# Performance work log

Hardware: AMD Instinct MI355X
Metric: run time of the kernel (lower is better)

Reference implementation:

```python
import jax, jax.numpy as jnp
import numpy as np

EMBED_DIM = 1024
B, T = 4, 2048

def setup_inputs() -> dict:
    key = jax.random.key(0)
    ks = jax.random.split(key, 7)
    s = 1.0 / np.sqrt(EMBED_DIM)
    return {
        "x": jax.random.normal(ks[0], (B, T, EMBED_DIM), dtype=jnp.float32),
        "Wq": jax.random.uniform(ks[1], (EMBED_DIM, EMBED_DIM), jnp.float32, -s, s),
        "bq": jax.random.uniform(ks[2], (EMBED_DIM,), jnp.float32, -s, s),
        "Wk": jax.random.uniform(ks[3], (EMBED_DIM, EMBED_DIM), jnp.float32, -s, s),
        "bk": jax.random.uniform(ks[4], (EMBED_DIM,), jnp.float32, -s, s),
        "Wv": jax.random.uniform(ks[5], (EMBED_DIM, EMBED_DIM), jnp.float32, -s, s),
        "bv": jax.random.uniform(ks[6], (EMBED_DIM,), jnp.float32, -s, s),
    }

def reference(x, Wq, bq, Wk, bk, Wv, bv):
    Bsz, Tlen, C = x.shape
    # torch Linear: y = x @ W.T + b
    Q = jnp.einsum('btc,dc->btd', x, Wq) + bq
    K = jnp.einsum('btc,dc->btd', x, Wk) + bk
    V = jnp.einsum('btc,dc->btd', x, Wv) + bv
    score = jnp.einsum('bqd,bkd->bqk', Q, K) / jnp.sqrt(jnp.float32(C))
    causal = jnp.tril(jnp.ones((Tlen, Tlen), dtype=bool))  # [T,T]
    score = jnp.where(causal, score, -jnp.inf)
    att = jax.nn.softmax(score, axis=-1)
    return jnp.einsum('bqk,bkd->bqd', att, V)
```

## Files before the change

### kernel.cpp

```cpp
#include <hip/hip_runtime.h>


using u16 = unsigned short;
typedef __attribute__((ext_vector_type(8))) short short8;
typedef __attribute__((ext_vector_type(4))) float f32x4;

__device__ __forceinline__ u16 f2b(float f) {
  unsigned u = __builtin_bit_cast(unsigned, f);
  u += 0x7fffu + ((u >> 16) & 1u);
  return (u16)(u >> 16);
}

__device__ __forceinline__ float b2f(u16 h) {
  return __builtin_bit_cast(float, (unsigned)h << 16);
}

__device__ __forceinline__ void async16(void* lds, const void* g) {
  __builtin_amdgcn_global_load_lds(
      (const __attribute__((address_space(1))) unsigned int*)g,
      (__attribute__((address_space(3))) unsigned int*)lds, 16, 0, 0);
}

__global__ __launch_bounds__(256) void cvt_all_kernel(
    const float* __restrict__ x, const float* __restrict__ Wq,
    const float* __restrict__ Wk, const float* __restrict__ Wv,
    u16* __restrict__ xb, u16* __restrict__ Wcat) {
  const int i = blockIdx.x * 256 + threadIdx.x;
  const float* src;
  u16* dst;
  int c;
  if (i < 2097152) {
    src = x; dst = xb; c = i;
  } else {
    const int r = i - 2097152;
    const int seg = r >> 18;
    src = seg == 0 ? Wq : (seg == 1 ? Wk : Wv);
    dst = Wcat + (size_t)seg * 1048576;
    c = r & 262143;
  }
  const float4 v = reinterpret_cast<const float4*>(src)[c];
  ushort4 o;
  o.x = f2b(v.x); o.y = f2b(v.y); o.z = f2b(v.z); o.w = f2b(v.w);
  reinterpret_cast<ushort4*>(dst)[c] = o;
}

template <typename Epi>
__device__ __forceinline__ void gemm_bt_tile(const u16* __restrict__ A, int lda,
                                             const u16* __restrict__ B, int ldb,
                                             int nt, Epi&& epi) {
  __shared__ __align__(16) u16 As[128 * 64];
  __shared__ __align__(16) u16 Bs[128 * 64];
  const int tid = threadIdx.x;
  const int lane = tid & 63;
  const int w = tid >> 6;
  const int wr = (w >> 1) << 6;
  const int wc = (w & 1) << 6;

  f32x4 acc[4][4];
#pragma unroll
  for (int i = 0; i < 4; ++i)
#pragma unroll
    for (int j = 0; j < 4; ++j) acc[i][j] = f32x4{0.f, 0.f, 0.f, 0.f};

  const int sr = tid >> 3;
  const int ce = ((tid & 7) ^ (sr & 7)) << 3;
  const u16* gA = A + (size_t)sr * lda + ce;
  const u16* gB = B + (size_t)sr * ldb + ce;
  u16* const dA = As + tid * 8;
  u16* const dB = Bs + tid * 8;

  const int hi = lane >> 4;
  const int lo7 = lane & 7;
  const int ra = (wr + (lane & 15)) << 6;
  const int rb = (wc + (lane & 15)) << 6;
  const int sk0 = (hi ^ lo7) << 3;
  const int sk1 = ((4 + hi) ^ lo7) << 3;

  for (int t = 0; t < nt; ++t) {
    __syncthreads();
#pragma unroll
    for (int s = 0; s < 4; ++s) {
      async16(dA + s * 2048, gA + (size_t)(s * 32) * lda);
      async16(dB + s * 2048, gB + (size_t)(s * 32) * ldb);
    }
    gA += 64;
    gB += 64;
    __syncthreads();
#pragma unroll
    for (int kk = 0; kk < 2; ++kk) {
      const int sk = kk ? sk1 : sk0;
      short8 af[4], bf[4];
#pragma unroll
      for (int i = 0; i < 4; ++i)
        af[i] = *(const short8*)(As + ra + i * 1024 + sk);
#pragma unroll
      for (int j = 0; j < 4; ++j)
        bf[j] = *(const short8*)(Bs + rb + j * 1024 + sk);
#pragma unroll
      for (int i = 0; i < 4; ++i)
#pragma unroll
        for (int j = 0; j < 4; ++j)
          acc[i][j] = __builtin_amdgcn_mfma_f32_16x16x32_bf16(af[i], bf[j],
                                                              acc[i][j], 0, 0, 0);
    }
  }
  epi(acc, wr, wc, lane);
}

__global__ __launch_bounds__(256) void qkv_kernel(
    const u16* __restrict__ xb, const u16* __restrict__ Wcat,
    const float* __restrict__ bq, const float* __restrict__ bk,
    const float* __restrict__ bv, u16* __restrict__ Qb, u16* __restrict__ Kb,
    u16* __restrict__ Vtb) {
  const int bid = blockIdx.x;
  const int z = bid >> 9;
  const int r = bid & 511;
  if (z < 2) {
    const int mt = r >> 3, nt = r & 7;
    const u16* W = Wcat + (size_t)z * 1048576;
    const float* bias = z ? bk : bq;
    u16* out = z ? Kb : Qb;
    const float scale = z ? 1.0f : 0.03125f;
    gemm_bt_tile(
        xb + (size_t)mt * 128 * 1024, 1024, W + (size_t)nt * 128 * 1024, 1024, 16,
        [&](f32x4(&acc)[4][4], int wr, int wc, int lane) {
          const int r0 = mt * 128 + wr + ((lane >> 4) << 2);
          const int c0 = nt * 128 + wc + (lane & 15);
#pragma unroll
          for (int i = 0; i < 4; ++i)
#pragma unroll
            for (int j = 0; j < 4; ++j) {
              const int col = c0 + j * 16;
              const float bb = bias[col];
#pragma unroll
              for (int rr = 0; rr < 4; ++rr)
                out[(size_t)(r0 + i * 16 + rr) * 1024 + col] =
                    f2b((acc[i][j][rr] + bb) * scale);
            }
        });
  } else {
    const int mt = r >> 6, nt = r & 63;
    const u16* Wvb = Wcat + (size_t)2 * 1048576;
    gemm_bt_tile(
        Wvb + (size_t)mt * 128 * 1024, 1024, xb + (size_t)nt * 128 * 1024, 1024, 16,
        [&](f32x4(&acc)[4][4], int wr, int wc, int lane) {
          const int r0 = mt * 128 + wr + ((lane >> 4) << 2);
          const int c0 = nt * 128 + wc + (lane & 15);
#pragma unroll
          for (int i = 0; i < 4; ++i)
#pragma unroll
            for (int rr = 0; rr < 4; ++rr) {
              const int row = r0 + i * 16 + rr;
              const float bb = bv[row];
#pragma unroll
              for (int j = 0; j < 4; ++j)
                Vtb[(size_t)row * 8192 + c0 + j * 16] = f2b(acc[i][j][rr] + bb);
            }
        });
  }
}

__global__ __launch_bounds__(256) void score_kernel(const u16* __restrict__ Qb,
                                                    const u16* __restrict__ Kb,
                                                    u16* __restrict__ S) {
  const int b = blockIdx.y;
  const int t = blockIdx.x;
  int qt = 0;
  while ((qt + 1) * (qt + 2) / 2 <= t) ++qt;
  const int kt = t - (qt * (qt + 1)) / 2;
  const u16* A = Qb + ((size_t)b * 2048 + qt * 128) * 1024;
  const u16* Bp = Kb + ((size_t)b * 2048 + kt * 128) * 1024;
  u16* Sb = S + (size_t)b * 2048 * 2048;
  gemm_bt_tile(A, 1024, Bp, 1024, 16,
               [&](f32x4(&acc)[4][4], int wr, int wc, int lane) {
                 const int r0 = qt * 128 + wr + ((lane >> 4) << 2);
                 const int c0 = kt * 128 + wc + (lane & 15);
#pragma unroll
                 for (int i = 0; i < 4; ++i)
#pragma unroll
                   for (int j = 0; j < 4; ++j)
#pragma unroll
                     for (int rr = 0; rr < 4; ++rr)
                       Sb[(size_t)(r0 + i * 16 + rr) * 2048 + c0 + j * 16] =
                           f2b(acc[i][j][rr]);
               });
}

__global__ __launch_bounds__(256) void softmax_kernel(const u16* __restrict__ S,
                                                      u16* __restrict__ P) {
  __shared__ float redm[4], reds[4];
  const int rowid = blockIdx.x;
  const int b = rowid >> 11;
  const int q = rowid & 2047;
  const u16* Srow = S + ((size_t)b * 2048 + q) * 2048;
  u16* Prow = P + ((size_t)b * 2048 + q) * 2048;
  const int L = q + 1;
  const int Lpad = ((q >> 7) + 1) << 7;
  const int tid = threadIdx.x;
  const int k0 = tid << 3;
  const bool active = k0 < Lpad;
  float v[8];
  float m = -1e30f;
  if (active) {
    const short8 s8 = *(const short8*)(Srow + k0);
#pragma unroll
    for (int j = 0; j < 8; ++j) {
      v[j] = (k0 + j < L) ? b2f((u16)s8[j]) : -1e30f;
      m = fmaxf(m, v[j]);
    }
  }
#pragma unroll
  for (int o = 32; o > 0; o >>= 1) m = fmaxf(m, __shfl_xor(m, o));
  if ((tid & 63) == 0) redm[tid >> 6] = m;
  __syncthreads();
  m = fmaxf(fmaxf(redm[0], redm[1]), fmaxf(redm[2], redm[3]));
  float s = 0.f;
  if (active) {
#pragma unroll
    for (int j = 0; j < 8; ++j) {
      const float e = (k0 + j < L) ? __expf(v[j] - m) : 0.f;
      v[j] = e;
      s += e;
    }
  }
#pragma unroll
  for (int o = 32; o > 0; o >>= 1) s += __shfl_xor(s, o);
  if ((tid & 63) == 0) reds[tid >> 6] = s;
  __syncthreads();
  s = reds[0] + reds[1] + reds[2] + reds[3];
  const float inv = 1.0f / s;
  if (active) {
    short8 o8;
#pragma unroll
    for (int j = 0; j < 8; ++j)
      o8[j] = (short)((k0 + j < L) ? f2b(v[j] * inv) : (u16)0);
    *(short8*)(Prow + k0) = o8;
  }
}

__global__ __launch_bounds__(256) void pv_kernel(const u16* __restrict__ P,
                                                 const u16* __restrict__ Vtb,
                                                 float* __restrict__ O) {
  const int bid = blockIdx.x;
  const int pair = bid >> 8;
  const int idx = bid & 255;
  const int hb = idx >> 7;
  const int qt_raw = (idx >> 3) & 15;
  const int dt = idx & 7;
  const int qt = pair ? (15 - qt_raw) : qt_raw;
  const int b = pair * 2 + hb;
  const u16* A = P + (size_t)b * 2048 * 2048 + (size_t)qt * 128 * 2048;
  const u16* Bp = Vtb + (size_t)dt * 128 * 8192 + b * 2048;
  float* Ob = O + (size_t)b * 2048 * 1024;
  gemm_bt_tile(A, 2048, Bp, 8192, (qt + 1) * 2,
               [&](f32x4(&acc)[4][4], int wr, int wc, int lane) {
                 const int r0 = qt * 128 + wr + ((lane >> 4) << 2);
                 const int c0 = dt * 128 + wc + (lane & 15);
#pragma unroll
                 for (int i = 0; i < 4; ++i)
#pragma unroll
                   for (int j = 0; j < 4; ++j)
#pragma unroll
                     for (int rr = 0; rr < 4; ++rr)
                       Ob[(size_t)(r0 + i * 16 + rr) * 1024 + c0 + j * 16] =
                           acc[i][j][rr];
               });
}

extern "C" void kernel_launch(void* const* d_in, const int* in_sizes, int n_in,
                              void* d_out, int out_size, void* d_ws, size_t ws_size,
                              hipStream_t stream) {
  const float* x = (const float*)d_in[0];
  const float* Wq = (const float*)d_in[1];
  const float* bq = (const float*)d_in[2];
  const float* Wk = (const float*)d_in[3];
  const float* bk = (const float*)d_in[4];
  const float* Wv = (const float*)d_in[5];
  const float* bv = (const float*)d_in[6];
  float* out = (float*)d_out;
  char* ws = (char*)d_ws;
  u16* Qb = (u16*)(ws);
  u16* Kb = (u16*)(ws + (16u << 20));
  u16* Vtb = (u16*)(ws + (32u << 20));
  u16* xb = (u16*)(ws + (48u << 20));
  u16* Wcat = (u16*)(ws + (64u << 20));
  u16* S = (u16*)(ws + (70u << 20));
  u16* P = (u16*)(ws + (134u << 20));

  cvt_all_kernel<<<11264, 256, 0, stream>>>(x, Wq, Wk, Wv, xb, Wcat);
  qkv_kernel<<<1536, 256, 0, stream>>>(xb, Wcat, bq, bk, bv, Qb, Kb, Vtb);
  score_kernel<<<dim3(136, 4), 256, 0, stream>>>(Qb, Kb, S);
  softmax_kernel<<<8192, 256, 0, stream>>>(S, P);
  pv_kernel<<<512, 256, 0, stream>>>(P, Vtb, out);
}
```

Before: 170.0 us.

## Double-buffer LDS tiles in QKV GEMM and remap blocks per XCD

Converts the QKV projection GEMM tile loop to a double-buffered LDS pipeline: the next K-slice is loaded asynchronously while MFMAs run on the current one, with explicit vmcnt waits and barriers. It also remaps block IDs so each XCD processes contiguous panels that share the same A rows, which should improve L2 reuse. The aim is to hide global-load latency and cut redundant DRAM traffic. In exchange LDS use per block doubles, which may lower occupancy.

New measurement: 218.7 us. 1.29x slower.

```diff
diff --git a/kernel.cpp b/kernel.cpp
--- a/kernel.cpp
+++ b/kernel.cpp
@@ -48,8 +48,8 @@
 __device__ __forceinline__ void gemm_bt_tile(const u16* __restrict__ A, int lda,
                                              const u16* __restrict__ B, int ldb,
                                              int nt, Epi&& epi) {
-  __shared__ __align__(16) u16 As[128 * 64];
-  __shared__ __align__(16) u16 Bs[128 * 64];
+  __shared__ __align__(16) u16 As[2][128 * 64];
+  __shared__ __align__(16) u16 Bs[2][128 * 64];
   const int tid = threadIdx.x;
   const int lane = tid & 63;
   const int w = tid >> 6;
@@ -66,8 +66,6 @@
   const int ce = ((tid & 7) ^ (sr & 7)) << 3;
   const u16* gA = A + (size_t)sr * lda + ce;
   const u16* gB = B + (size_t)sr * ldb + ce;
-  u16* const dA = As + tid * 8;
-  u16* const dB = Bs + tid * 8;
 
   const int hi = lane >> 4;
   const int lo7 = lane & 7;
@@ -76,26 +74,31 @@
   const int sk0 = (hi ^ lo7) << 3;
   const int sk1 = ((4 + hi) ^ lo7) << 3;
 
-  for (int t = 0; t < nt; ++t) {
-    __syncthreads();
+  auto stage = [&](int buf, int t) {
+    u16* const dA = As[buf] + tid * 8;
+    u16* const dB = Bs[buf] + tid * 8;
+    const u16* ga = gA + t * 64;
+    const u16* gb = gB + t * 64;
 #pragma unroll
     for (int s = 0; s < 4; ++s) {
-      async16(dA + s * 2048, gA + (size_t)(s * 32) * lda);
-      async16(dB + s * 2048, gB + (size_t)(s * 32) * ldb);
+      async16(dA + s * 2048, ga + (size_t)(s * 32) * lda);
+      async16(dB + s * 2048, gb + (size_t)(s * 32) * ldb);
     }
-    gA += 64;
-    gB += 64;
-    __syncthreads();
+  };
+
+  auto compute = [&](int buf) {
+    const u16* const Ab = As[buf];
+    const u16* const Bb = Bs[buf];
 #pragma unroll
     for (int kk = 0; kk < 2; ++kk) {
       const int sk = kk ? sk1 : sk0;
       short8 af[4], bf[4];
 #pragma unroll
       for (int i = 0; i < 4; ++i)
-        af[i] = *(const short8*)(As + ra + i * 1024 + sk);
+        af[i] = *(const short8*)(Ab + ra + i * 1024 + sk);
 #pragma unroll
       for (int j = 0; j < 4; ++j)
-        bf[j] = *(const short8*)(Bs + rb + j * 1024 + sk);
+        bf[j] = *(const short8*)(Bb + rb + j * 1024 + sk);
 #pragma unroll
       for (int i = 0; i < 4; ++i)
 #pragma unroll
@@ -103,7 +106,22 @@
           acc[i][j] = __builtin_amdgcn_mfma_f32_16x16x32_bf16(af[i], bf[j],
                                                               acc[i][j], 0, 0, 0);
     }
-  }
+  };
+
+  stage(0, 0);
+  int cur = 0;
+  for (int t = 0; t < nt - 1; ++t) {
+    stage(cur ^ 1, t + 1);
+    asm volatile("s_waitcnt vmcnt(8)" ::: "memory");
+    __builtin_amdgcn_s_barrier();
+    compute(cur);
+    asm volatile("s_waitcnt lgkmcnt(0)" ::: "memory");
+    __builtin_amdgcn_s_barrier();
+    cur ^= 1;
+  }
+  asm volatile("s_waitcnt vmcnt(0)" ::: "memory");
+  __builtin_amdgcn_s_barrier();
+  compute(cur);
   epi(acc, wr, wc, lane);
 }
 
@@ -113,10 +131,14 @@
     const float* __restrict__ bv, u16* __restrict__ Qb, u16* __restrict__ Kb,
     u16* __restrict__ Vtb) {
   const int bid = blockIdx.x;
-  const int z = bid >> 9;
-  const int r = bid & 511;
-  if (z < 2) {
-    const int mt = r >> 3, nt = r & 7;
+  const int xcd = bid & 7;
+  const int u = bid >> 3;
+  const int panel = xcd * 24 + (u >> 3);
+  const int unit = u & 7;
+  if (panel < 128) {
+    const int z = panel >> 6;
+    const int mt = panel & 63;
+    const int nt = unit;
     const u16* W = Wcat + (size_t)z * 1048576;
     const float* bias = z ? bk : bq;
     u16* out = z ? Kb : Qb;
@@ -139,7 +161,8 @@
             }
         });
   } else {
-    const int mt = r >> 6, nt = r & 63;
+    const int nt = panel - 128;
+    const int mt = unit;
     const u16* Wvb = Wcat + (size_t)2 * 1048576;
     gemm_bt_tile(
         Wvb + (size_t)mt * 128 * 1024, 1024, xb + (size_t)nt * 128 * 1024, 1024, 16,
```

## Split QKV into 256x256 8-phase pipelined QK GEMM and separate V kernel

Applied to the files above, without the earlier changes.

The Q and K projections move to a new 256x256-tile GEMM with 512 threads, double-buffered async global-to-LDS loads, XOR-swizzled LDS, and an 8-phase schedule. That schedule interleaves LDS reads, staging and MFMA quads with barriers and setprio. The V projection becomes its own kernel with a remapped block order for cache locality, and the QK grid is also swizzled. The aim is higher MFMA utilisation and more reuse per tile, at the cost of one extra kernel launch, one block per CU, and heavy register pressure from 32 accumulators.

After: 162.4 us. 4.4% less time.

```diff
diff --git a/kernel.cpp b/kernel.cpp
--- a/kernel.cpp
+++ b/kernel.cpp
@@ -19,6 +19,12 @@
   __builtin_amdgcn_global_load_lds(
       (const __attribute__((address_space(1))) unsigned int*)g,
       (__attribute__((address_space(3))) unsigned int*)lds, 16, 0, 0);
+}
+
+__device__ __forceinline__ void block_barrier() {
+  asm volatile("" ::: "memory");
+  __builtin_amdgcn_s_barrier();
+  asm volatile("" ::: "memory");
 }
 
 __global__ __launch_bounds__(256) void cvt_all_kernel(
@@ -44,6 +50,147 @@
   reinterpret_cast<ushort4*>(dst)[c] = o;
 }
 
+#define STG_A(buf, half, roff, ku)                                          \
+  {                                                                         \
+    async16(&Asm[buf][half][tid * 8], gA0 + (size_t)(roff)*lda + (ku));     \
+    async16(&Asm[buf][half][4096 + tid * 8],                                \
+            gA0 + (size_t)((roff) + 128) * lda + (ku));                     \
+  }
+#define STG_B(buf, half, roff, ku)                                          \
+  {                                                                         \
+    async16(&Bsm[buf][half][tid * 8], gB0 + (size_t)(roff)*ldb + (ku));     \
+    async16(&Bsm[buf][half][4096 + tid * 8],                                \
+            gB0 + (size_t)((roff) + 128) * ldb + (ku));                     \
+  }
+#define RD_A(buf, hh)                                                       \
+  {                                                                         \
+    _Pragma("unroll") for (int ii = 0; ii < 4; ++ii) {                      \
+      a[ii][0] = *(const short8*)(&Asm[buf][hh][aoff + ii * 1024 + sk0]);   \
+      a[ii][1] = *(const short8*)(&Asm[buf][hh][aoff + ii * 1024 + sk1]);   \
+    }                                                                       \
+  }
+#define RD_B(buf, cc, breg)                                                 \
+  {                                                                         \
+    _Pragma("unroll") for (int jj = 0; jj < 2; ++jj) {                      \
+      breg[jj][0] = *(const short8*)(&Bsm[buf][cc][boff + jj * 1024 + sk0]);\
+      breg[jj][1] = *(const short8*)(&Bsm[buf][cc][boff + jj * 1024 + sk1]);\
+    }                                                                       \
+  }
+#define QUAD(hh, cc, breg)                                                  \
+  {                                                                         \
+    __builtin_amdgcn_s_setprio(1);                                          \
+    _Pragma("unroll") for (int ii = 0; ii < 4; ++ii)                        \
+        _Pragma("unroll") for (int jj = 0; jj < 2; ++jj) {                  \
+      acc[(hh)*4 + ii][(cc)*2 + jj] =                                       \
+          __builtin_amdgcn_mfma_f32_16x16x32_bf16(                          \
+              a[ii][0], breg[jj][0], acc[(hh)*4 + ii][(cc)*2 + jj], 0,0,0); \
+      acc[(hh)*4 + ii][(cc)*2 + jj] =                                       \
+          __builtin_amdgcn_mfma_f32_16x16x32_bf16(                          \
+              a[ii][1], breg[jj][1], acc[(hh)*4 + ii][(cc)*2 + jj], 0,0,0); \
+    }                                                                       \
+    __builtin_amdgcn_s_setprio(0);                                          \
+  }
+#define LGK0 asm volatile("s_waitcnt lgkmcnt(0)" ::: "memory")
+#define VM6 asm volatile("s_waitcnt vmcnt(6)" ::: "memory")
+
+template <int NT, typename Epi>
+__device__ __forceinline__ void gemm256_8ph(const u16* __restrict__ A, int lda,
+                                            const u16* __restrict__ B, int ldb,
+                                            Epi&& epi) {
+  __shared__ __align__(16) u16 Asm[2][2][8192];
+  __shared__ __align__(16) u16 Bsm[2][2][8192];
+  const int tid = threadIdx.x;
+  const int lane = tid & 63;
+  const int w = tid >> 6;
+  const int wm = w >> 2;
+  const int wn = w & 3;
+
+  f32x4 acc[8][4];
+#pragma unroll
+  for (int i = 0; i < 8; ++i)
+#pragma unroll
+    for (int j = 0; j < 4; ++j) acc[i][j] = f32x4{0.f, 0.f, 0.f, 0.f};
+
+  const int sr = tid >> 3;
+  const int ce = ((tid & 7) ^ (sr & 7)) << 3;
+  const u16* gA0 = A + (size_t)sr * lda + ce;
+  const int bE = (sr & 31) + ((sr >> 5) << 6);
+  const u16* gB0 = B + (size_t)bE * ldb + ce;
+
+  const int l15 = lane & 15;
+  const int hi = lane >> 4;
+  const int lo7 = lane & 7;
+  const int aoff = wm * 4096 + l15 * 64;
+  const int boff = wn * 2048 + l15 * 64;
+  const int sk0 = (hi ^ lo7) << 3;
+  const int sk1 = ((4 + hi) ^ lo7) << 3;
+
+  short8 a[4][2], bEr[2][2], bLr[2][2];
+
+  STG_A(0, 0, 0, 0); STG_B(0, 0, 0, 0); STG_A(0, 1, 64, 0); STG_B(0, 1, 32, 0);
+  STG_A(1, 0, 0, 64); STG_B(1, 0, 0, 64); STG_A(1, 1, 64, 64);
+  VM6;
+  block_barrier();
+
+  for (int t = 0; t < NT; t += 2) {
+    const int k1 = (t + 1) * 64;
+    const int t2c = (t + 2 < NT) ? (t + 2) : (NT - 1);
+    const int t3c = (t + 3 < NT) ? (t + 3) : (NT - 1);
+    const int k2 = t2c * 64;
+    const int k3 = t3c * 64;
+    RD_A(0, 0); RD_B(0, 0, bEr); STG_B(1, 1, 32, k1);
+    block_barrier(); LGK0; QUAD(0, 0, bEr); block_barrier();
+    RD_B(0, 1, bLr); STG_A(0, 0, 0, k2);
+    block_barrier(); LGK0; QUAD(0, 1, bLr); block_barrier();
+    RD_A(0, 1); STG_B(0, 0, 0, k2);
+    block_barrier(); LGK0; QUAD(1, 1, bLr); block_barrier();
+    STG_A(0, 1, 64, k2);
+    VM6; block_barrier(); QUAD(1, 0, bEr); block_barrier();
+    RD_A(1, 0); RD_B(1, 0, bEr); STG_B(0, 1, 32, k2);
+    block_barrier(); LGK0; QUAD(0, 0, bEr); block_barrier();
+    RD_B(1, 1, bLr); STG_A(1, 0, 0, k3);
+    block_barrier(); LGK0; QUAD(0, 1, bLr); block_barrier();
+    RD_A(1, 1); STG_B(1, 0, 0, k3);
+    block_barrier(); LGK0; QUAD(1, 1, bLr); block_barrier();
+    STG_A(1, 1, 64, k3);
+    VM6; block_barrier(); QUAD(1, 0, bEr); block_barrier();
+  }
+  asm volatile("s_waitcnt vmcnt(0)" ::: "memory");
+  epi(acc, wm, wn, lane);
+}
+
+__global__ __launch_bounds__(512, 1) void qkv_qk_kernel(
+    const u16* __restrict__ xb, const u16* __restrict__ Wcat,
+    const float* __restrict__ bq, const float* __restrict__ bk,
+    u16* __restrict__ Qb, u16* __restrict__ Kb) {
+  const int bid = blockIdx.x;
+  const int swz = (bid & 7) * 32 + (bid >> 3);
+  const int mt = swz >> 3, nt = swz & 7;
+  const int z = nt >> 2;
+  const float* bias = z ? bk : bq;
+  u16* out = z ? Kb : Qb;
+  const float scale = z ? 1.0f : 0.03125f;
+  gemm256_8ph<16>(
+      xb + (size_t)mt * 256 * 1024, 1024, Wcat + (size_t)nt * 256 * 1024, 1024,
+      [&](f32x4(&acc)[8][4], int wm, int wn, int lane) {
+        const int r0 = mt * 256 + wm * 128 + ((lane >> 4) << 2);
+        const int c0 = (nt & 3) * 256 + wn * 64 + (lane & 15);
+#pragma unroll
+        for (int i8 = 0; i8 < 8; ++i8) {
+          const int rb = r0 + (i8 >> 2) * 64 + (i8 & 3) * 16;
+#pragma unroll
+          for (int i4 = 0; i4 < 4; ++i4) {
+            const int col = c0 + (i4 >> 1) * 32 + (i4 & 1) * 16;
+            const float bb = bias[col];
+#pragma unroll
+            for (int rr = 0; rr < 4; ++rr)
+              out[(size_t)(rb + rr) * 1024 + col] =
+                  f2b((acc[i8][i4][rr] + bb) * scale);
+          }
+        }
+      });
+}
+
 template <typename Epi>
 __device__ __forceinline__ void gemm_bt_tile(const u16* __restrict__ A, int lda,
                                              const u16* __restrict__ B, int ldb,
@@ -107,57 +254,30 @@
   epi(acc, wr, wc, lane);
 }
 
-__global__ __launch_bounds__(256) void qkv_kernel(
+__global__ __launch_bounds__(256) void qkv_v_kernel(
     const u16* __restrict__ xb, const u16* __restrict__ Wcat,
-    const float* __restrict__ bq, const float* __restrict__ bk,
-    const float* __restrict__ bv, u16* __restrict__ Qb, u16* __restrict__ Kb,
-    u16* __restrict__ Vtb) {
+    const float* __restrict__ bv, u16* __restrict__ Vtb) {
   const int bid = blockIdx.x;
-  const int z = bid >> 9;
-  const int r = bid & 511;
-  if (z < 2) {
-    const int mt = r >> 3, nt = r & 7;
-    const u16* W = Wcat + (size_t)z * 1048576;
-    const float* bias = z ? bk : bq;
-    u16* out = z ? Kb : Qb;
-    const float scale = z ? 1.0f : 0.03125f;
-    gemm_bt_tile(
-        xb + (size_t)mt * 128 * 1024, 1024, W + (size_t)nt * 128 * 1024, 1024, 16,
-        [&](f32x4(&acc)[4][4], int wr, int wc, int lane) {
-          const int r0 = mt * 128 + wr + ((lane >> 4) << 2);
-          const int c0 = nt * 128 + wc + (lane & 15);
-#pragma unroll
-          for (int i = 0; i < 4; ++i)
-#pragma unroll
-            for (int j = 0; j < 4; ++j) {
-              const int col = c0 + j * 16;
-              const float bb = bias[col];
-#pragma unroll
-              for (int rr = 0; rr < 4; ++rr)
-                out[(size_t)(r0 + i * 16 + rr) * 1024 + col] =
-                    f2b((acc[i][j][rr] + bb) * scale);
-            }
-        });
-  } else {
-    const int mt = r >> 6, nt = r & 63;
-    const u16* Wvb = Wcat + (size_t)2 * 1048576;
-    gemm_bt_tile(
-        Wvb + (size_t)mt * 128 * 1024, 1024, xb + (size_t)nt * 128 * 1024, 1024, 16,
-        [&](f32x4(&acc)[4][4], int wr, int wc, int lane) {
-          const int r0 = mt * 128 + wr + ((lane >> 4) << 2);
-          const int c0 = nt * 128 + wc + (lane & 15);
-#pragma unroll
-          for (int i = 0; i < 4; ++i)
-#pragma unroll
-            for (int rr = 0; rr < 4; ++rr) {
-              const int row = r0 + i * 16 + rr;
-              const float bb = bv[row];
-#pragma unroll
-              for (int j = 0; j < 4; ++j)
-                Vtb[(size_t)row * 8192 + c0 + j * 16] = f2b(acc[i][j][rr] + bb);
-            }
-        });
-  }
+  const int u = bid >> 3;
+  const int nt = (bid & 7) * 8 + (u >> 3);
+  const int mt = u & 7;
+  const u16* Wvb = Wcat + (size_t)2 * 1048576;
+  gemm_bt_tile(
+      Wvb + (size_t)mt * 128 * 1024, 1024, xb + (size_t)nt * 128 * 1024, 1024, 16,
+      [&](f32x4(&acc)[4][4], int wr, int wc, int lane) {
+        const int r0 = mt * 128 + wr + ((lane >> 4) << 2);
+        const int c0 = nt * 128 + wc + (lane & 15);
+#pragma unroll
+        for (int i = 0; i < 4; ++i)
+#pragma unroll
+          for (int rr = 0; rr < 4; ++rr) {
+            const int row = r0 + i * 16 + rr;
+            const float bb = bv[row];
+#pragma unroll
+            for (int j = 0; j < 4; ++j)
+              Vtb[(size_t)row * 8192 + c0 + j * 16] = f2b(acc[i][j][rr] + bb);
+          }
+      });
 }
 
 __global__ __launch_bounds__(256) void score_kernel(const u16* __restrict__ Qb,
@@ -288,7 +408,8 @@
   u16* P = (u16*)(ws + (134u << 20));
 
   cvt_all_kernel<<<11264, 256, 0, stream>>>(x, Wq, Wk, Wv, xb, Wcat);
-  qkv_kernel<<<1536, 256, 0, stream>>>(xb, Wcat, bq, bk, bv, Qb, Kb, Vtb);
+  qkv_qk_kernel<<<256, 512, 0, stream>>>(xb, Wcat, bq, bk, Qb, Kb);
+  qkv_v_kernel<<<512, 256, 0, stream>>>(xb, Wcat, bv, Vtb);
   score_kernel<<<dim3(136, 4), 256, 0, stream>>>(Qb, Kb, S);
   softmax_kernel<<<8192, 256, 0, stream>>>(S, P);
   pv_kernel<<<512, 256, 0, stream>>>(P, Vtb, out);
```
